# Performance work log

Hardware: AMD Instinct MI355X
Metric: run time of the kernel (lower is better)

The kernel has to match this reference:

```python
import jax, jax.numpy as jnp
import numpy as np

N_USERS = 100000
N_ITEMS = 50000
NNZ = 1600000
DIM = 64


def setup_inputs() -> dict:
    key = jax.random.key(0)
    k1, k2, k3, k4, k5, k6, k7 = jax.random.split(key, 7)
    user_x = jax.random.normal(k1, (N_USERS, DIM), dtype=jnp.float32)
    item_x = jax.random.normal(k2, (N_ITEMS, DIM), dtype=jnp.float32)
    # Xavier-uniform-like init for the two weight matrices
    limit = float(np.sqrt(6.0 / (DIM + DIM)))
    user_weight = jax.random.uniform(k3, (DIM, DIM), jnp.float32, -limit, limit)
    item_weight = jax.random.uniform(k4, (DIM, DIM), jnp.float32, -limit, limit)
    # Bipartite adjacency in COO form: ui_graph[r, c] = v ; iu_graph is its transpose
    ui_rows = jax.random.randint(k5, (NNZ,), 0, N_USERS, dtype=jnp.int32)
    ui_cols = jax.random.randint(k6, (NNZ,), 0, N_ITEMS, dtype=jnp.int32)
    ui_vals = jax.random.uniform(k7, (NNZ,), dtype=jnp.float32)
    return {
        "user_x": user_x,
        "item_x": item_x,
        "user_weight": user_weight,
        "item_weight": item_weight,
        "ui_rows": ui_rows,
        "ui_cols": ui_cols,
        "ui_vals": ui_vals,
    }


def _spmm(rows, cols, vals, dense, num_segments):
    # sparse[rows, cols] @ dense  -> gather source rows, scale, scatter-add to dest
    msgs = vals[:, None] * dense[cols]                      # [nnz, d]
    return jax.ops.segment_sum(msgs, rows, num_segments=num_segments)


def reference(user_x, item_x, user_weight, item_weight, ui_rows, ui_cols, ui_vals):
    # dropout p=0.0 -> identity (module default)
    xw_user = user_x @ user_weight                          # [n_users, d]
    xw_item = item_x @ item_weight                          # [n_items, d]
    # out_user = ui_graph @ xw_item ; out_item = iu_graph @ xw_user (iu = ui^T)
    out_user = _spmm(ui_rows, ui_cols, ui_vals, xw_item, N_USERS)
    out_item = _spmm(ui_cols, ui_rows, ui_vals, xw_user, N_ITEMS)
    return jax.nn.relu(out_user), jax.nn.relu(out_item)
```

## Files before the change

kernel.cpp:

```cpp
#include <hip/hip_runtime.h>
#include <hip/hip_bf16.h>

#define N_USERS 100000
#define N_ITEMS 50000
#define NNZ_EDGES 1600000
#define DIM 64

#define BSHIFT_U 7
#define BD_U 128
#define BSHIFT_I 6
#define BD_I 64
#define NBU ((N_USERS + BD_U - 1) / BD_U)
#define NBI ((N_ITEMS + BD_I - 1) / BD_I)
#define NB_MAX 782
#define TILE 4096
#define CAP 2432
#define GEMM_BLKS_U ((N_USERS + 63) / 64)
#define GEMM_BLKS_I ((N_ITEMS + 63) / 64)


__device__ inline unsigned short f32_to_bf16(float f) {
  unsigned u = __float_as_uint(f);
  unsigned r = (u + 0x7FFFu + ((u >> 16) & 1u)) >> 16;
  return (unsigned short)r;
}
__device__ inline float bf16_to_f32(unsigned short h) {
  return __uint_as_float((unsigned)h << 16);
}

__global__ __launch_bounds__(256) void gemm_both_kernel(
    const float* __restrict__ Xu, const float* __restrict__ Wu,
    unsigned short* __restrict__ Yu,
    const float* __restrict__ Xi, const float* __restrict__ Wi,
    unsigned short* __restrict__ Yi,
    int* __restrict__ cur_u, int* __restrict__ cur_i) {
  __shared__ float sXT[64][64];
  __shared__ float sW[64][64];
  const int tid = threadIdx.x;

  if (blockIdx.x == 0) {
    for (int t = tid; t < NBU; t += 256) cur_u[t] = t * CAP;
    for (int t = tid; t < NBI; t += 256) cur_i[t] = t * CAP;
  }

  const float* X; const float* W; unsigned short* Y; int nrows, row_base;
  if (blockIdx.x < GEMM_BLKS_U) {
    X = Xu; W = Wu; Y = Yu; nrows = N_USERS; row_base = blockIdx.x * 64;
  } else {
    X = Xi; W = Wi; Y = Yi; nrows = N_ITEMS; row_base = (blockIdx.x - GEMM_BLKS_U) * 64;
  }

  {
    const float4* Wv = (const float4*)W;
    float4* sWv = (float4*)&sW[0][0];
    #pragma unroll
    for (int i = 0; i < 4; ++i) sWv[tid + i * 256] = Wv[tid + i * 256];
  }
  {
    const int r = tid & 63;
    const int k0 = (tid >> 6) * 16;
    const int grow = row_base + r;
    #pragma unroll
    for (int i = 0; i < 4; ++i) {
      float4 v = make_float4(0.f, 0.f, 0.f, 0.f);
      if (grow < nrows) v = ((const float4*)(X + (size_t)grow * DIM + k0))[i];
      sXT[k0 + i * 4 + 0][r] = v.x;
      sXT[k0 + i * 4 + 1][r] = v.y;
      sXT[k0 + i * 4 + 2][r] = v.z;
      sXT[k0 + i * 4 + 3][r] = v.w;
    }
  }
  __syncthreads();

  const int tx = tid & 15;
  const int ty = tid >> 4;
  float acc[4][4] = {{0.f}};

  #pragma unroll 8
  for (int k = 0; k < 64; ++k) {
    const float4 a = *(const float4*)&sXT[k][ty * 4];
    const float4 b = *(const float4*)&sW[k][tx * 4];
    acc[0][0] = fmaf(a.x, b.x, acc[0][0]);
    acc[0][1] = fmaf(a.x, b.y, acc[0][1]);
    acc[0][2] = fmaf(a.x, b.z, acc[0][2]);
    acc[0][3] = fmaf(a.x, b.w, acc[0][3]);
    acc[1][0] = fmaf(a.y, b.x, acc[1][0]);
    acc[1][1] = fmaf(a.y, b.y, acc[1][1]);
    acc[1][2] = fmaf(a.y, b.z, acc[1][2]);
    acc[1][3] = fmaf(a.y, b.w, acc[1][3]);
    acc[2][0] = fmaf(a.z, b.x, acc[2][0]);
    acc[2][1] = fmaf(a.z, b.y, acc[2][1]);
    acc[2][2] = fmaf(a.z, b.z, acc[2][2]);
    acc[2][3] = fmaf(a.z, b.w, acc[2][3]);
    acc[3][0] = fmaf(a.w, b.x, acc[3][0]);
    acc[3][1] = fmaf(a.w, b.y, acc[3][1]);
    acc[3][2] = fmaf(a.w, b.z, acc[3][2]);
    acc[3][3] = fmaf(a.w, b.w, acc[3][3]);
  }

  #pragma unroll
  for (int r = 0; r < 4; ++r) {
    const int grow = row_base + ty * 4 + r;
    if (grow < nrows) {
      ushort4 o;
      o.x = f32_to_bf16(acc[r][0]);
      o.y = f32_to_bf16(acc[r][1]);
      o.z = f32_to_bf16(acc[r][2]);
      o.w = f32_to_bf16(acc[r][3]);
      *(ushort4*)(Y + (size_t)grow * DIM + tx * 4) = o;
    }
  }
}

__global__ __launch_bounds__(1024) void binning2_kernel(
    const int* __restrict__ rows, const int* __restrict__ cols,
    const float* __restrict__ vals,
    int* __restrict__ cur_u, int* __restrict__ cur_i,
    uint2* __restrict__ out_u, uint2* __restrict__ out_i, int nnz) {
  __shared__ int sh[NB_MAX];
  __shared__ int scnt[NB_MAX];
  __shared__ uint2 sbuf[TILE];
  __shared__ unsigned short sbk[TILE];
  __shared__ int s_w[16];

  const int tid = threadIdx.x, lane = tid & 63, wid = tid >> 6;
  const int tbase = blockIdx.x * TILE;
  const int total = min(TILE, nnz - tbase);

  int er[4], ec[4]; unsigned ev[4];
  #pragma unroll
  for (int k = 0; k < 4; ++k) {
    const int i = tbase + k * 1024 + tid;
    if (i < nnz) {
      er[k] = rows[i];
      ec[k] = cols[i];
      ev[k] = __float_as_uint(vals[i]);
    } else {
      er[k] = -1; ec[k] = 0; ev[k] = 0;
    }
  }

#define BIN_PHASE(BKEXPR, PKEXPR, NB, CUR, OUT)                                \
  {                                                                            \
    for (int j = tid; j < (NB); j += 1024) sh[j] = 0;                          \
    __syncthreads();                                                           \
    int bk[4]; unsigned pk[4];                                                 \
    _Pragma("unroll")                                                          \
    for (int k = 0; k < 4; ++k) {                                              \
      if (er[k] >= 0) {                                                        \
        bk[k] = (BKEXPR); pk[k] = (PKEXPR);                                    \
        atomicAdd(&sh[bk[k]], 1);                                              \
      } else { bk[k] = -1; pk[k] = 0; }                                        \
    }                                                                          \
    __syncthreads();                                                           \
    {                                                                          \
      const int x = (tid < (NB)) ? sh[tid] : 0;                                \
      int incl = x;                                                            \
      _Pragma("unroll")                                                        \
      for (int d = 1; d < 64; d <<= 1) {                                       \
        int t = __shfl_up(incl, d);                                            \
        if (lane >= d) incl += t;                                              \
      }                                                                        \
      if (lane == 63) s_w[wid] = incl;                                         \
      __syncthreads();                                                         \
      if (tid == 0) {                                                          \
        int a = 0;                                                             \
        _Pragma("unroll")                                                      \
        for (int w = 0; w < 16; ++w) { const int t = s_w[w]; s_w[w] = a; a += t; } \
      }                                                                        \
      __syncthreads();                                                         \
      const int excl = s_w[wid] + incl - x;                                    \
      if (tid < (NB)) { scnt[tid] = x; sh[tid] = excl; }                       \
      __syncthreads();                                                         \
    }                                                                          \
    _Pragma("unroll")                                                          \
    for (int k = 0; k < 4; ++k) {                                              \
      if (bk[k] >= 0) {                                                        \
        const int p = atomicAdd(&sh[bk[k]], 1);                                \
        sbuf[p] = make_uint2(pk[k], ev[k]);                                    \
        sbk[p] = (unsigned short)bk[k];                                        \
      }                                                                        \
    }                                                                          \
    __syncthreads();                                                           \
    if (tid < (NB)) {                                                          \
      const int c = scnt[tid];                                                 \
      const int excl = sh[tid] - c;                                            \
      int g = 0;                                                               \
      if (c > 0) g = atomicAdd(&(CUR)[tid], c);                                \
      scnt[tid] = excl;                                                        \
      sh[tid] = g;                                                             \
    }                                                                          \
    __syncthreads();                                                           \
    for (int p = tid; p < total; p += 1024) {                                  \
      const int b = sbk[p];                                                    \
      (OUT)[sh[b] + (p - scnt[b])] = sbuf[p];                                  \
    }                                                                          \
    __syncthreads();                                                           \
  }

  BIN_PHASE(er[k] >> BSHIFT_U,
            ((unsigned)(er[k] & (BD_U - 1)) << 24) | ((unsigned)ec[k] << 6),
            NBU, cur_u, out_u)
  BIN_PHASE(ec[k] >> BSHIFT_I,
            ((unsigned)(ec[k] & (BD_I - 1)) << 24) | ((unsigned)er[k] << 6),
            NBI, cur_i, out_i)
#undef BIN_PHASE
}

__global__ __launch_bounds__(512) void sort_spmm_kernel(
    const uint2* __restrict__ bin_u, const int* __restrict__ cur_u,
    const unsigned short* __restrict__ xw_item, float* __restrict__ out_user,
    const uint2* __restrict__ bin_i, const int* __restrict__ cur_i,
    const unsigned short* __restrict__ xw_user, float* __restrict__ out_item) {
  __shared__ uint2 sbuf[CAP];
  __shared__ int cnt[128];
  __shared__ int roff[128];
  __shared__ int s_w[2];
  const int tid = threadIdx.x;
  const int lane = tid & 63, wid = tid >> 6;

  const uint2* bin; const int* cur; const unsigned short* xw; float* out;
  int b, bd, ndst;
  if (blockIdx.x < NBU) {
    b = blockIdx.x; bd = BD_U; ndst = N_USERS;
    bin = bin_u; cur = cur_u; xw = xw_item; out = out_user;
  } else {
    b = blockIdx.x - NBU; bd = BD_I; ndst = N_ITEMS;
    bin = bin_i; cur = cur_i; xw = xw_user; out = out_item;
  }
  const int beg = b * CAP;
  const int n = min(cur[b] - beg, CAP);

  if (tid < bd) cnt[tid] = 0;
  __syncthreads();

  uint2 rg[5];
  #pragma unroll
  for (int k = 0; k < 5; ++k) {
    const int i = k * 512 + tid;
    if (i < n) {
      rg[k] = bin[beg + i];
      atomicAdd(&cnt[rg[k].x >> 24], 1);
    } else {
      rg[k] = make_uint2(0u, 0u);
    }
  }
  __syncthreads();

  int x = 0, incl = 0;
  if (tid < 128) {
    x = (tid < bd) ? cnt[tid] : 0;
    incl = x;
    #pragma unroll
    for (int d = 1; d < 64; d <<= 1) {
      int t = __shfl_up(incl, d);
      if (lane >= d) incl += t;
    }
    if (lane == 63) s_w[wid] = incl;
  }
  __syncthreads();
  if (tid == 0) {
    const int t0 = s_w[0];
    s_w[0] = 0;
    s_w[1] = t0;
  }
  __syncthreads();
  if (tid < 128) {
    const int excl = s_w[wid] + incl - x;
    if (tid < bd) {
      roff[tid] = excl;
      cnt[tid] = excl;
    }
  }
  __syncthreads();

  #pragma unroll
  for (int k = 0; k < 5; ++k) {
    const int i = k * 512 + tid;
    if (i < n) {
      const int p = atomicAdd(&cnt[rg[k].x >> 24], 1);
      sbuf[p] = rg[k];
    }
  }
  __syncthreads();

  const unsigned short* __restrict__ xwl = xw + lane;
  for (int r = wid; r < bd; r += 8) {
    const int rb = roff[r], re = cnt[r];
    float acc = 0.f;
    int j = rb;
    for (; j + 16 <= re; j += 16) {
      uint2 e[16];
      #pragma unroll
      for (int q = 0; q < 16; ++q) e[q] = sbuf[j + q];
      unsigned short h[16];
      #pragma unroll
      for (int q = 0; q < 16; ++q) h[q] = xwl[e[q].x & 0xFFFFC0u];
      #pragma unroll
      for (int q = 0; q < 16; ++q)
        acc = fmaf(__uint_as_float(e[q].y), bf16_to_f32(h[q]), acc);
    }
    for (; j + 8 <= re; j += 8) {
      uint2 e[8];
      #pragma unroll
      for (int q = 0; q < 8; ++q) e[q] = sbuf[j + q];
      unsigned short h[8];
      #pragma unroll
      for (int q = 0; q < 8; ++q) h[q] = xwl[e[q].x & 0xFFFFC0u];
      #pragma unroll
      for (int q = 0; q < 8; ++q)
        acc = fmaf(__uint_as_float(e[q].y), bf16_to_f32(h[q]), acc);
    }
    for (; j + 4 <= re; j += 4) {
      uint2 e[4];
      #pragma unroll
      for (int q = 0; q < 4; ++q) e[q] = sbuf[j + q];
      unsigned short h[4];
      #pragma unroll
      for (int q = 0; q < 4; ++q) h[q] = xwl[e[q].x & 0xFFFFC0u];
      #pragma unroll
      for (int q = 0; q < 4; ++q)
        acc = fmaf(__uint_as_float(e[q].y), bf16_to_f32(h[q]), acc);
    }
    for (; j < re; ++j) {
      const uint2 e = sbuf[j];
      acc = fmaf(__uint_as_float(e.y), bf16_to_f32(xwl[e.x & 0xFFFFC0u]), acc);
    }
    const int grow = b * bd + r;
    if (grow < ndst) out[(size_t)grow * DIM + lane] = fmaxf(acc, 0.f);
  }
}

extern "C" void kernel_launch(void* const* d_in, const int* in_sizes, int n_in,
                              void* d_out, int out_size, void* d_ws, size_t ws_size,
                              hipStream_t stream) {
  const float* user_x      = (const float*)d_in[0];
  const float* item_x      = (const float*)d_in[1];
  const float* user_weight = (const float*)d_in[2];
  const float* item_weight = (const float*)d_in[3];
  const int*   ui_rows     = (const int*)d_in[4];
  const int*   ui_cols     = (const int*)d_in[5];
  const float* ui_vals     = (const float*)d_in[6];

  float* out_user = (float*)d_out;
  float* out_item = (float*)d_out + (size_t)N_USERS * DIM;

  unsigned short* xw_user = (unsigned short*)d_ws;
  unsigned short* xw_item = xw_user + (size_t)N_USERS * DIM;
  uint2* binA = (uint2*)(xw_item + (size_t)N_ITEMS * DIM);
  uint2* binB = binA + (size_t)NBU * CAP;
  int*   cur_u = (int*)(binB + (size_t)NBI * CAP);
  int*   cur_i = cur_u + NBU;

  gemm_both_kernel<<<GEMM_BLKS_U + GEMM_BLKS_I, 256, 0, stream>>>(
      user_x, user_weight, xw_user, item_x, item_weight, xw_item, cur_u, cur_i);

  const int nblk = (NNZ_EDGES + TILE - 1) / TILE;
  binning2_kernel<<<nblk, 1024, 0, stream>>>(ui_rows, ui_cols, ui_vals,
                                             cur_u, cur_i, binA, binB, NNZ_EDGES);

  sort_spmm_kernel<<<NBU + NBI, 512, 0, stream>>>(
      binA, cur_u, xw_item, out_user,
      binB, cur_i, xw_user, out_item);
}
```

Baseline: 117.5 us.

## Fuse GEMM and edge binning into one prep kernel with memset-initialized cursors

The separate GEMM and binning kernels are merged into one launch: the first blocks compute X·W for 128 rows each, and the remaining blocks bin edges using 512 threads over 8 edges per thread. The bin cursors are now zeroed with a memset instead of being set to t*CAP inside the GEMM kernel, which lets binning run concurrently with the GEMM. The packed edge key is shifted so the column index becomes a direct byte offset. This removes one kernel boundary and lets the two independent phases overlap. In exchange it adds a memset node and uses a larger, shared-memory-heavy block type that may limit occupancy for the GEMM blocks.

```diff
diff --git a/kernel.cpp b/kernel.cpp
--- a/kernel.cpp
+++ b/kernel.cpp
@@ -15,8 +15,10 @@
 #define NB_MAX 782
 #define TILE 4096
 #define CAP 2432
-#define GEMM_BLKS_U ((N_USERS + 63) / 64)
-#define GEMM_BLKS_I ((N_ITEMS + 63) / 64)
+
+#define PREP_GU ((N_USERS + 127) / 128)
+#define PREP_GI ((N_ITEMS + 127) / 128)
+#define PREP_BIN ((NNZ_EDGES + TILE - 1) / TILE)
 
 
 __device__ inline unsigned short f32_to_bf16(float f) {
@@ -28,110 +30,111 @@
   return __uint_as_float((unsigned)h << 16);
 }
 
-__global__ __launch_bounds__(256) void gemm_both_kernel(
+__global__ __launch_bounds__(512) void prep_kernel(
     const float* __restrict__ Xu, const float* __restrict__ Wu,
     unsigned short* __restrict__ Yu,
     const float* __restrict__ Xi, const float* __restrict__ Wi,
     unsigned short* __restrict__ Yi,
-    int* __restrict__ cur_u, int* __restrict__ cur_i) {
-  __shared__ float sXT[64][64];
-  __shared__ float sW[64][64];
-  const int tid = threadIdx.x;
-
-  if (blockIdx.x == 0) {
-    for (int t = tid; t < NBU; t += 256) cur_u[t] = t * CAP;
-    for (int t = tid; t < NBI; t += 256) cur_i[t] = t * CAP;
-  }
-
-  const float* X; const float* W; unsigned short* Y; int nrows, row_base;
-  if (blockIdx.x < GEMM_BLKS_U) {
-    X = Xu; W = Wu; Y = Yu; nrows = N_USERS; row_base = blockIdx.x * 64;
-  } else {
-    X = Xi; W = Wi; Y = Yi; nrows = N_ITEMS; row_base = (blockIdx.x - GEMM_BLKS_U) * 64;
-  }
-
-  {
-    const float4* Wv = (const float4*)W;
-    float4* sWv = (float4*)&sW[0][0];
-    #pragma unroll
-    for (int i = 0; i < 4; ++i) sWv[tid + i * 256] = Wv[tid + i * 256];
-  }
-  {
-    const int r = tid & 63;
-    const int k0 = (tid >> 6) * 16;
-    const int grow = row_base + r;
-    #pragma unroll
-    for (int i = 0; i < 4; ++i) {
-      float4 v = make_float4(0.f, 0.f, 0.f, 0.f);
-      if (grow < nrows) v = ((const float4*)(X + (size_t)grow * DIM + k0))[i];
-      sXT[k0 + i * 4 + 0][r] = v.x;
-      sXT[k0 + i * 4 + 1][r] = v.y;
-      sXT[k0 + i * 4 + 2][r] = v.z;
-      sXT[k0 + i * 4 + 3][r] = v.w;
-    }
-  }
-  __syncthreads();
-
-  const int tx = tid & 15;
-  const int ty = tid >> 4;
-  float acc[4][4] = {{0.f}};
-
-  #pragma unroll 8
-  for (int k = 0; k < 64; ++k) {
-    const float4 a = *(const float4*)&sXT[k][ty * 4];
-    const float4 b = *(const float4*)&sW[k][tx * 4];
-    acc[0][0] = fmaf(a.x, b.x, acc[0][0]);
-    acc[0][1] = fmaf(a.x, b.y, acc[0][1]);
-    acc[0][2] = fmaf(a.x, b.z, acc[0][2]);
-    acc[0][3] = fmaf(a.x, b.w, acc[0][3]);
-    acc[1][0] = fmaf(a.y, b.x, acc[1][0]);
-    acc[1][1] = fmaf(a.y, b.y, acc[1][1]);
-    acc[1][2] = fmaf(a.y, b.z, acc[1][2]);
-    acc[1][3] = fmaf(a.y, b.w, acc[1][3]);
-    acc[2][0] = fmaf(a.z, b.x, acc[2][0]);
-    acc[2][1] = fmaf(a.z, b.y, acc[2][1]);
-    acc[2][2] = fmaf(a.z, b.z, acc[2][2]);
-    acc[2][3] = fmaf(a.z, b.w, acc[2][3]);
-    acc[3][0] = fmaf(a.w, b.x, acc[3][0]);
-    acc[3][1] = fmaf(a.w, b.y, acc[3][1]);
-    acc[3][2] = fmaf(a.w, b.z, acc[3][2]);
-    acc[3][3] = fmaf(a.w, b.w, acc[3][3]);
-  }
-
-  #pragma unroll
-  for (int r = 0; r < 4; ++r) {
-    const int grow = row_base + ty * 4 + r;
-    if (grow < nrows) {
-      ushort4 o;
-      o.x = f32_to_bf16(acc[r][0]);
-      o.y = f32_to_bf16(acc[r][1]);
-      o.z = f32_to_bf16(acc[r][2]);
-      o.w = f32_to_bf16(acc[r][3]);
-      *(ushort4*)(Y + (size_t)grow * DIM + tx * 4) = o;
-    }
-  }
-}
-
-__global__ __launch_bounds__(1024) void binning2_kernel(
     const int* __restrict__ rows, const int* __restrict__ cols,
     const float* __restrict__ vals,
     int* __restrict__ cur_u, int* __restrict__ cur_i,
-    uint2* __restrict__ out_u, uint2* __restrict__ out_i, int nnz) {
-  __shared__ int sh[NB_MAX];
-  __shared__ int scnt[NB_MAX];
-  __shared__ uint2 sbuf[TILE];
-  __shared__ unsigned short sbk[TILE];
-  __shared__ int s_w[16];
-
+    uint2* __restrict__ out_u, uint2* __restrict__ out_i) {
+  __shared__ char smem[49152];
   const int tid = threadIdx.x, lane = tid & 63, wid = tid >> 6;
-  const int tbase = blockIdx.x * TILE;
-  const int total = min(TILE, nnz - tbase);
-
-  int er[4], ec[4]; unsigned ev[4];
+
+  if (blockIdx.x < PREP_GU + PREP_GI) {
+    float* sW = (float*)smem;
+    float* sXTb = (float*)(smem + 16384);
+    const int sub = tid >> 8;
+    const int stid = tid & 255;
+
+    const float* X; const float* W; unsigned short* Y; int nrows, row_base;
+    if (blockIdx.x < PREP_GU) {
+      X = Xu; W = Wu; Y = Yu; nrows = N_USERS;
+      row_base = blockIdx.x * 128 + sub * 64;
+    } else {
+      X = Xi; W = Wi; Y = Yi; nrows = N_ITEMS;
+      row_base = (blockIdx.x - PREP_GU) * 128 + sub * 64;
+    }
+
+    {
+      const float4* Wv = (const float4*)W;
+      float4* sWv = (float4*)sW;
+      #pragma unroll
+      for (int i = 0; i < 2; ++i) sWv[tid + i * 512] = Wv[tid + i * 512];
+    }
+    float* sXT = sXTb + sub * 64 * 64;
+    {
+      const int r = stid & 63;
+      const int k0 = (stid >> 6) * 16;
+      const int grow = row_base + r;
+      #pragma unroll
+      for (int i = 0; i < 4; ++i) {
+        float4 v = make_float4(0.f, 0.f, 0.f, 0.f);
+        if (grow < nrows) v = ((const float4*)(X + (size_t)grow * DIM + k0))[i];
+        sXT[(k0 + i * 4 + 0) * 64 + r] = v.x;
+        sXT[(k0 + i * 4 + 1) * 64 + r] = v.y;
+        sXT[(k0 + i * 4 + 2) * 64 + r] = v.z;
+        sXT[(k0 + i * 4 + 3) * 64 + r] = v.w;
+      }
+    }
+    __syncthreads();
+
+    const int tx = stid & 15;
+    const int ty = stid >> 4;
+    float acc[4][4] = {{0.f}};
+
+    #pragma unroll 8
+    for (int k = 0; k < 64; ++k) {
+      const float4 a = *(const float4*)&sXT[k * 64 + ty * 4];
+      const float4 b = *(const float4*)&sW[k * 64 + tx * 4];
+      acc[0][0] = fmaf(a.x, b.x, acc[0][0]);
+      acc[0][1] = fmaf(a.x, b.y, acc[0][1]);
+      acc[0][2] = fmaf(a.x, b.z, acc[0][2]);
+      acc[0][3] = fmaf(a.x, b.w, acc[0][3]);
+      acc[1][0] = fmaf(a.y, b.x, acc[1][0]);
+      acc[1][1] = fmaf(a.y, b.y, acc[1][1]);
+      acc[1][2] = fmaf(a.y, b.z, acc[1][2]);
+      acc[1][3] = fmaf(a.y, b.w, acc[1][3]);
+      acc[2][0] = fmaf(a.z, b.x, acc[2][0]);
+      acc[2][1] = fmaf(a.z, b.y, acc[2][1]);
+      acc[2][2] = fmaf(a.z, b.z, acc[2][2]);
+      acc[2][3] = fmaf(a.z, b.w, acc[2][3]);
+      acc[3][0] = fmaf(a.w, b.x, acc[3][0]);
+      acc[3][1] = fmaf(a.w, b.y, acc[3][1]);
+      acc[3][2] = fmaf(a.w, b.z, acc[3][2]);
+      acc[3][3] = fmaf(a.w, b.w, acc[3][3]);
+    }
+
+    #pragma unroll
+    for (int r = 0; r < 4; ++r) {
+      const int grow = row_base + ty * 4 + r;
+      if (grow < nrows) {
+        ushort4 o;
+        o.x = f32_to_bf16(acc[r][0]);
+        o.y = f32_to_bf16(acc[r][1]);
+        o.z = f32_to_bf16(acc[r][2]);
+        o.w = f32_to_bf16(acc[r][3]);
+        *(ushort4*)(Y + (size_t)grow * DIM + tx * 4) = o;
+      }
+    }
+    return;
+  }
+
+  uint2* sbuf = (uint2*)smem;
+  unsigned short* sbk = (unsigned short*)(smem + 32768);
+  int* sh   = (int*)(smem + 40960);
+  int* scnt = (int*)(smem + 44088);
+  int* s_w  = (int*)(smem + 47232);
+
+  const int tbase = (blockIdx.x - (PREP_GU + PREP_GI)) * TILE;
+  const int total = min(TILE, NNZ_EDGES - tbase);
+
+  int er[8], ec[8]; unsigned ev[8];
   #pragma unroll
-  for (int k = 0; k < 4; ++k) {
-    const int i = tbase + k * 1024 + tid;
-    if (i < nnz) {
+  for (int k = 0; k < 8; ++k) {
+    const int i = tbase + k * 512 + tid;
+    if (i < NNZ_EDGES) {
       er[k] = rows[i];
       ec[k] = cols[i];
       ev[k] = __float_as_uint(vals[i]);
@@ -142,19 +145,21 @@
 
 #define BIN_PHASE(BKEXPR, PKEXPR, NB, CUR, OUT)                                \
   {                                                                            \
-    for (int j = tid; j < (NB); j += 1024) sh[j] = 0;                          \
-    __syncthreads();                                                           \
-    int bk[4]; unsigned pk[4];                                                 \
+    for (int j = tid; j < (NB); j += 512) sh[j] = 0;                           \
+    __syncthreads();                                                           \
+    int bk[8]; unsigned pk[8];                                                 \
     _Pragma("unroll")                                                          \
-    for (int k = 0; k < 4; ++k) {                                              \
+    for (int k = 0; k < 8; ++k) {                                              \
       if (er[k] >= 0) {                                                        \
         bk[k] = (BKEXPR); pk[k] = (PKEXPR);                                    \
         atomicAdd(&sh[bk[k]], 1);                                              \
       } else { bk[k] = -1; pk[k] = 0; }                                        \
     }                                                                          \
     __syncthreads();                                                           \
-    {                                                                          \
-      const int x = (tid < (NB)) ? sh[tid] : 0;                                \
+    int carry = 0;                                                             \
+    for (int cb = 0; cb < (NB); cb += 512) {                                   \
+      const int idx = cb + tid;                                                \
+      const int x = (idx < (NB)) ? sh[idx] : 0;                                \
       int incl = x;                                                            \
       _Pragma("unroll")                                                        \
       for (int d = 1; d < 64; d <<= 1) {                                       \
@@ -166,15 +171,17 @@
       if (tid == 0) {                                                          \
         int a = 0;                                                             \
         _Pragma("unroll")                                                      \
-        for (int w = 0; w < 16; ++w) { const int t = s_w[w]; s_w[w] = a; a += t; } \
+        for (int w = 0; w < 8; ++w) { const int t = s_w[w]; s_w[w] = a; a += t; } \
+        s_w[8] = a;                                                            \
       }                                                                        \
       __syncthreads();                                                         \
-      const int excl = s_w[wid] + incl - x;                                    \
-      if (tid < (NB)) { scnt[tid] = x; sh[tid] = excl; }                       \
+      const int excl = carry + s_w[wid] + incl - x;                            \
+      if (idx < (NB)) { scnt[idx] = x; sh[idx] = excl; }                       \
+      carry += s_w[8];                                                         \
       __syncthreads();                                                         \
     }                                                                          \
     _Pragma("unroll")                                                          \
-    for (int k = 0; k < 4; ++k) {                                              \
+    for (int k = 0; k < 8; ++k) {                                              \
       if (bk[k] >= 0) {                                                        \
         const int p = atomicAdd(&sh[bk[k]], 1);                                \
         sbuf[p] = make_uint2(pk[k], ev[k]);                                    \
@@ -182,16 +189,16 @@
       }                                                                        \
     }                                                                          \
     __syncthreads();                                                           \
-    if (tid < (NB)) {                                                          \
-      const int c = scnt[tid];                                                 \
-      const int excl = sh[tid] - c;                                            \
+    for (int idx = tid; idx < (NB); idx += 512) {                              \
+      const int c = scnt[idx];                                                 \
+      const int excl = sh[idx] - c;                                            \
       int g = 0;                                                               \
-      if (c > 0) g = atomicAdd(&(CUR)[tid], c);                                \
-      scnt[tid] = excl;                                                        \
-      sh[tid] = g;                                                             \
-    }                                                                          \
-    __syncthreads();                                                           \
-    for (int p = tid; p < total; p += 1024) {                                  \
+      if (c > 0) g = atomicAdd(&(CUR)[idx], c);                                \
+      scnt[idx] = excl;                                                        \
+      sh[idx] = idx * CAP + g;                                                 \
+    }                                                                          \
+    __syncthreads();                                                           \
+    for (int p = tid; p < total; p += 512) {                                   \
       const int b = sbk[p];                                                    \
       (OUT)[sh[b] + (p - scnt[b])] = sbuf[p];                                  \
     }                                                                          \
@@ -199,10 +206,10 @@
   }
 
   BIN_PHASE(er[k] >> BSHIFT_U,
-            ((unsigned)(er[k] & (BD_U - 1)) << 24) | ((unsigned)ec[k] << 6),
+            ((unsigned)(er[k] & (BD_U - 1)) << 25) | ((unsigned)ec[k] << 7),
             NBU, cur_u, out_u)
   BIN_PHASE(ec[k] >> BSHIFT_I,
-            ((unsigned)(ec[k] & (BD_I - 1)) << 24) | ((unsigned)er[k] << 6),
+            ((unsigned)(ec[k] & (BD_I - 1)) << 25) | ((unsigned)er[k] << 7),
             NBI, cur_i, out_i)
 #undef BIN_PHASE
 }
@@ -229,7 +236,7 @@
     bin = bin_i; cur = cur_i; xw = xw_user; out = out_item;
   }
   const int beg = b * CAP;
-  const int n = min(cur[b] - beg, CAP);
+  const int n = min(cur[b], CAP);
 
   if (tid < bd) cnt[tid] = 0;
   __syncthreads();
@@ -240,7 +247,7 @@
     const int i = k * 512 + tid;
     if (i < n) {
       rg[k] = bin[beg + i];
-      atomicAdd(&cnt[rg[k].x >> 24], 1);
+      atomicAdd(&cnt[rg[k].x >> 25], 1);
     } else {
       rg[k] = make_uint2(0u, 0u);
     }
@@ -278,13 +285,13 @@
   for (int k = 0; k < 5; ++k) {
     const int i = k * 512 + tid;
     if (i < n) {
-      const int p = atomicAdd(&cnt[rg[k].x >> 24], 1);
+      const int p = atomicAdd(&cnt[rg[k].x >> 25], 1);
       sbuf[p] = rg[k];
     }
   }
   __syncthreads();
 
-  const unsigned short* __restrict__ xwl = xw + lane;
+  const char* __restrict__ xwb = (const char*)xw + lane * 2;
   for (int r = wid; r < bd; r += 8) {
     const int rb = roff[r], re = cnt[r];
     float acc = 0.f;
@@ -295,7 +302,8 @@
       for (int q = 0; q < 16; ++q) e[q] = sbuf[j + q];
       unsigned short h[16];
       #pragma unroll
-      for (int q = 0; q < 16; ++q) h[q] = xwl[e[q].x & 0xFFFFC0u];
+      for (int q = 0; q < 16; ++q)
+        h[q] = *(const unsigned short*)(xwb + (e[q].x & 0x01FFFF80u));
       #pragma unroll
       for (int q = 0; q < 16; ++q)
         acc = fmaf(__uint_as_float(e[q].y), bf16_to_f32(h[q]), acc);
@@ -306,7 +314,8 @@
       for (int q = 0; q < 8; ++q) e[q] = sbuf[j + q];
       unsigned short h[8];
       #pragma unroll
-      for (int q = 0; q < 8; ++q) h[q] = xwl[e[q].x & 0xFFFFC0u];
+      for (int q = 0; q < 8; ++q)
+        h[q] = *(const unsigned short*)(xwb + (e[q].x & 0x01FFFF80u));
       #pragma unroll
       for (int q = 0; q < 8; ++q)
         acc = fmaf(__uint_as_float(e[q].y), bf16_to_f32(h[q]), acc);
@@ -317,14 +326,17 @@
       for (int q = 0; q < 4; ++q) e[q] = sbuf[j + q];
       unsigned short h[4];
       #pragma unroll
-      for (int q = 0; q < 4; ++q) h[q] = xwl[e[q].x & 0xFFFFC0u];
+      for (int q = 0; q < 4; ++q)
+        h[q] = *(const unsigned short*)(xwb + (e[q].x & 0x01FFFF80u));
       #pragma unroll
       for (int q = 0; q < 4; ++q)
         acc = fmaf(__uint_as_float(e[q].y), bf16_to_f32(h[q]), acc);
     }
     for (; j < re; ++j) {
       const uint2 e = sbuf[j];
-      acc = fmaf(__uint_as_float(e.y), bf16_to_f32(xwl[e.x & 0xFFFFC0u]), acc);
+      acc = fmaf(__uint_as_float(e.y),
+                 bf16_to_f32(*(const unsigned short*)(xwb + (e.x & 0x01FFFF80u))),
+                 acc);
     }
     const int grow = b * bd + r;
     if (grow < ndst) out[(size_t)grow * DIM + lane] = fmaxf(acc, 0.f);
@@ -352,12 +364,11 @@
   int*   cur_u = (int*)(binB + (size_t)NBI * CAP);
   int*   cur_i = cur_u + NBU;
 
-  gemm_both_kernel<<<GEMM_BLKS_U + GEMM_BLKS_I, 256, 0, stream>>>(
-      user_x, user_weight, xw_user, item_x, item_weight, xw_item, cur_u, cur_i);
-
-  const int nblk = (NNZ_EDGES + TILE - 1) / TILE;
-  binning2_kernel<<<nblk, 1024, 0, stream>>>(ui_rows, ui_cols, ui_vals,
-                                             cur_u, cur_i, binA, binB, NNZ_EDGES);
+  hipMemsetAsync(cur_u, 0, (NBU + NBI) * sizeof(int), stream);
+
+  prep_kernel<<<PREP_GU + PREP_GI + PREP_BIN, 512, 0, stream>>>(
+      user_x, user_weight, xw_user, item_x, item_weight, xw_item,
+      ui_rows, ui_cols, ui_vals, cur_u, cur_i, binA, binB);
 
   sort_spmm_kernel<<<NBU + NBI, 512, 0, stream>>>(
       binA, cur_u, xw_item, out_user,
```

Measured after the change: 110.9 us. 1.06x faster.
